# Kernel optimization log

Measured on AMD Instinct MI355X. Metric: run time of the kernel, lower is better.

Reference implementation:

```python
import jax, jax.numpy as jnp
import numpy as np

B, L, DEPTH, W = 32, 256, 4, 32

def setup_inputs() -> dict:
    key = jax.random.key(0)
    ks = jax.random.split(key, 12)
    rn = lambda k, sh: jax.random.normal(k, sh, dtype=jnp.float32)
    return {
        "x": rn(ks[0], (B, L, L)),
        "ai": rn(ks[1], (W, 1)),
        "ao": rn(ks[2], (1, W)),
        "a": rn(ks[3], (DEPTH, W, W)),
        "bi": rn(ks[4], (W, 1)),
        "bo": rn(ks[5], (1, W)),
        "b": rn(ks[6], (DEPTH, W, W)),
        "ci": rn(ks[7], (W, 1)),
        "co": rn(ks[8], (1, W)),
        "c": rn(ks[9], (DEPTH, W, W)),
        "bias_i": rn(ks[10], (W,)),
        "bias": rn(ks[11], (DEPTH, W)),
    }

def _layer(x, wc, wb, wa, bias):
    # x: [b, ci, X, Y]; wc/wb/wa: [co, ci]; circular 3x3 stencil via rolls
    y = jnp.einsum('oi,bixy->boxy', wc, x)
    nb = (jnp.roll(x, 1, axis=2) + jnp.roll(x, -1, axis=2)
          + jnp.roll(x, 1, axis=3) + jnp.roll(x, -1, axis=3))
    y = y + jnp.einsum('oi,bixy->boxy', wb, nb)
    dg = (jnp.roll(x, (1, 1), axis=(2, 3)) + jnp.roll(x, (-1, -1), axis=(2, 3))
          + jnp.roll(x, (1, -1), axis=(2, 3)) + jnp.roll(x, (-1, 1), axis=(2, 3)))
    y = y + jnp.einsum('oi,bixy->boxy', wa, dg)
    if bias is not None:
        y = y + bias[None, :, None, None]
    return y

def _act(x):
    # torch nn.GELU() default is exact (erf-based)
    return jax.nn.gelu(x, approximate=False)

def _func(x, ai, ao, a, bi, bo, b, ci, co, c, bias_i, bias):
    h = x[:, None, :, :]                       # [b,1,L,L]
    h = _act(_layer(h, ci, bi, ai, bias_i))    # [b,W,L,L]
    for k in range(a.shape[0]):
        h = _act(_layer(h, c[k], b[k], a[k], bias[k]))
    y = _layer(h, co, bo, ao, None)            # [b,1,L,L]
    return jnp.squeeze(y, axis=1)              # [b,L,L]

def reference(x, ai, ao, a, bi, bo, b, ci, co, c, bias_i, bias):
    f = lambda v: _func(v, ai, ao, a, bi, bo, b, ci, co, c, bias_i, bias)
    return 0.5 * (f(x) - f(-x))
```

## Files before the change

### kernel.cpp

```cpp
#include <hip/hip_runtime.h>
#include <hip/hip_bf16.h>

#define B_ 32
#define L_ 256
#define W_ 32
#define TILE 16
#define PSTR 40
#define LL (L_*L_)

typedef float    floatx4 __attribute__((ext_vector_type(4)));
typedef short    shortx8 __attribute__((ext_vector_type(8)));
typedef unsigned uintx2  __attribute__((ext_vector_type(2)));
typedef unsigned uintx4  __attribute__((ext_vector_type(4)));

__device__ __forceinline__ float gelu_fast(float x) {
    float x2 = x * x;
    float inner = fmaf(0.044715f * x2, x, x);
    float e = __builtin_amdgcn_exp2f(inner * -2.3022082299446597f);
    return x * __builtin_amdgcn_rcpf(1.0f + e);
}

#if __has_builtin(__builtin_amdgcn_cvt_pk_bf16_f32)
__device__ __forceinline__ unsigned pack_bf2(float a, float b) {
    auto v = __builtin_amdgcn_cvt_pk_bf16_f32(a, b);
    return __builtin_bit_cast(unsigned, v);
}
#else
__device__ __forceinline__ unsigned pack_bf2(float a, float b) {
    unsigned ua = __float_as_uint(a);
    unsigned ub = __float_as_uint(b);
    ua += 0x7fffu + ((ua >> 16) & 1u);
    ub += 0x7fffu + ((ub >> 16) & 1u);
    return (ua >> 16) | (ub & 0xffff0000u);
}
#endif

__device__ __forceinline__ int swizzle_blk(int p) {
    return (p & 7) * 1024 + (p >> 3);
}

__device__ __forceinline__ void conv9(
        const shortx8& t00, const shortx8& t01, const shortx8& t02,
        const shortx8& t10, const shortx8& t11, const shortx8& t12,
        const shortx8& t20, const shortx8& t21, const shortx8& t22,
        const shortx8 af[3][2], const float bv[2][4], floatx4 acc[2]) {
    #pragma unroll
    for (int h = 0; h < 2; ++h) {
        acc[h] = floatx4{bv[h][0], bv[h][1], bv[h][2], bv[h][3]};
        acc[h] = __builtin_amdgcn_mfma_f32_16x16x32_bf16(af[0][h], t11, acc[h], 0, 0, 0);
        acc[h] = __builtin_amdgcn_mfma_f32_16x16x32_bf16(af[1][h], t01, acc[h], 0, 0, 0);
        acc[h] = __builtin_amdgcn_mfma_f32_16x16x32_bf16(af[1][h], t21, acc[h], 0, 0, 0);
        acc[h] = __builtin_amdgcn_mfma_f32_16x16x32_bf16(af[1][h], t10, acc[h], 0, 0, 0);
        acc[h] = __builtin_amdgcn_mfma_f32_16x16x32_bf16(af[1][h], t12, acc[h], 0, 0, 0);
        acc[h] = __builtin_amdgcn_mfma_f32_16x16x32_bf16(af[2][h], t00, acc[h], 0, 0, 0);
        acc[h] = __builtin_amdgcn_mfma_f32_16x16x32_bf16(af[2][h], t02, acc[h], 0, 0, 0);
        acc[h] = __builtin_amdgcn_mfma_f32_16x16x32_bf16(af[2][h], t20, acc[h], 0, 0, 0);
        acc[h] = __builtin_amdgcn_mfma_f32_16x16x32_bf16(af[2][h], t22, acc[h], 0, 0, 0);
    }
}

__device__ __forceinline__ void gelu_pack4(const floatx4 acc[2], unsigned d[4]) {
    d[0] = pack_bf2(gelu_fast(acc[0][0]), gelu_fast(acc[0][1]));
    d[1] = pack_bf2(gelu_fast(acc[0][2]), gelu_fast(acc[0][3]));
    d[2] = pack_bf2(gelu_fast(acc[1][0]), gelu_fast(acc[1][1]));
    d[3] = pack_bf2(gelu_fast(acc[1][2]), gelu_fast(acc[1][3]));
}

__device__ __forceinline__ void build_afrag(
        const float* wc, const float* wb, const float* wa, const float* bias,
        int m, int q, shortx8 af[3][2], float bv[2][4]) {
    const float* wm[3] = { wc, wb, wa };
    #pragma unroll
    for (int f = 0; f < 3; ++f)
      #pragma unroll
      for (int h = 0; h < 2; ++h) {
        const float* row = wm[f] + (h*16 + m) * W_ + q*8;
        floatx4 r0 = *(const floatx4*)(row);
        floatx4 r1 = *(const floatx4*)(row + 4);
        union { shortx8 s; unsigned u[4]; } w;
        w.u[0] = pack_bf2(r0.x, r0.y);
        w.u[1] = pack_bf2(r0.z, r0.w);
        w.u[2] = pack_bf2(r1.x, r1.y);
        w.u[3] = pack_bf2(r1.z, r1.w);
        af[f][h] = w.s;
      }
    #pragma unroll
    for (int h = 0; h < 2; ++h)
      #pragma unroll
      for (int r = 0; r < 4; ++r)
        bv[h][r] = bias[h*16 + q*4 + r];
}

__global__ __launch_bounds__(256) void kern_first(
        const float* __restrict__ x, float scale,
        const float* __restrict__ ci, const float* __restrict__ bi,
        const float* __restrict__ ai, const float* __restrict__ bias_i,
        unsigned short* __restrict__ hout) {
    __shared__ float tile[18*18];
    __shared__ float wC[W_], wB[W_], wA[W_], bs[W_];
    int blk = swizzle_blk(blockIdx.x);
    int b = blk >> 8;
    int t = blk & 255;
    int x0 = (t >> 4) * TILE;
    int y0 = (t & 15) * TILE;
    int tid = threadIdx.x;
    if (tid < W_) { wC[tid] = ci[tid]; wB[tid] = bi[tid]; wA[tid] = ai[tid]; bs[tid] = bias_i[tid]; }
    const float* xb = x + (size_t)b * LL;
    for (int idx = tid; idx < 18*18; idx += 256) {
        int dy = idx / 18, dx = idx % 18;
        int gx = (x0 + dy - 1) & 255;
        int gy = (y0 + dx - 1) & 255;
        tile[idx] = scale * xb[gx * L_ + gy];
    }
    __syncthreads();
    int dx = tid & 15, dy = tid >> 4;
    const float* c0 = &tile[dy * 18 + dx];
    float ctr = c0[19];
    float nb  = c0[1] + c0[37] + c0[18] + c0[20];
    float dg  = c0[0] + c0[2] + c0[36] + c0[38];
    unsigned od[16];
    #pragma unroll
    for (int o = 0; o < 16; ++o) {
        float v0 = gelu_fast(wC[2*o]*ctr + wB[2*o]*nb + wA[2*o]*dg + bs[2*o]);
        float v1 = gelu_fast(wC[2*o+1]*ctr + wB[2*o+1]*nb + wA[2*o+1]*dg + bs[2*o+1]);
        od[o] = pack_bf2(v0, v1);
    }
    unsigned* dst = (unsigned*)(hout + (((((size_t)b << 8) | (unsigned)(x0+dy)) << 8 | (unsigned)(y0+dx)) << 5));
    *(uintx4*)(dst)      = uintx4{od[0],  od[1],  od[2],  od[3]};
    *(uintx4*)(dst + 4)  = uintx4{od[4],  od[5],  od[6],  od[7]};
    *(uintx4*)(dst + 8)  = uintx4{od[8],  od[9],  od[10], od[11]};
    *(uintx4*)(dst + 12) = uintx4{od[12], od[13], od[14], od[15]};
}

__global__ __launch_bounds__(256, 4) void kern_mid2(
        const unsigned short* __restrict__ hin,
        const float* __restrict__ wc1, const float* __restrict__ wb1,
        const float* __restrict__ wa1, const float* __restrict__ bias1,
        const float* __restrict__ wc2, const float* __restrict__ wb2,
        const float* __restrict__ wa2, const float* __restrict__ bias2,
        unsigned short* __restrict__ hout) {
    __shared__ unsigned short tile2[400 * PSTR];

    const int tid = threadIdx.x;
    const int blk = swizzle_blk(blockIdx.x);
    const int b  = blk >> 8;
    const int t  = blk & 255;
    const int x0 = (t >> 4) * TILE;
    const int y0 = (t & 15) * TILE;

    const unsigned short* hb = hin + ((size_t)b << 21);

    #pragma unroll
    for (int jj = 0; jj < 7; ++jj) {
        int j = tid + jj * 256;
        if (j < 1600) {
            int qtr = j & 3;
            int pos = j >> 2;
            int r = (pos * 3277) >> 16;
            int c = pos - r * 20;
            int gx = (x0 + r - 2) & 255;
            int gy = (y0 + c - 2) & 255;
            shortx8 v = *(const shortx8*)(hb + ((((unsigned)gx << 8) | (unsigned)gy) << 5) + qtr*8);
            *(shortx8*)(tile2 + pos * PSTR + qtr * 8) = v;
        }
    }

    const int lane = tid & 63;
    const int wv   = tid >> 6;
    const int m    = lane & 15;
    const int q    = lane >> 4;

    shortx8 afrag[3][2];
    float bv[2][4];
    build_afrag(wc1, wb1, wa1, bias1, m, q, afrag, bv);

    __syncthreads();

#define LDT(tr, off) (*(const shortx8*)(tile2 + (((tr)*20 + m + (off)))*PSTR + q*8))

    const int trow0 = wv * 4;
    shortx8 W[3][3];
    #pragma unroll
    for (int i = 0; i < 3; ++i) {
        W[i][0] = LDT(trow0 + i, 0);
        W[i][1] = LDT(trow0 + i, 1);
        W[i][2] = LDT(trow0 + i, 2);
    }
    unsigned heldA[2][4];
    #pragma unroll
    for (int rr = 0; rr < 4; ++rr) {
        const int top = rr % 3, mid = (rr + 1) % 3, bot = (rr + 2) % 3;
        floatx4 acc[2];
        conv9(W[top][0], W[top][1], W[top][2],
              W[mid][0], W[mid][1], W[mid][2],
              W[bot][0], W[bot][1], W[bot][2], afrag, bv, acc);
        unsigned d[4];
        gelu_pack4(acc, d);
        if (rr < 2) {
            heldA[rr][0] = d[0]; heldA[rr][1] = d[1];
            heldA[rr][2] = d[2]; heldA[rr][3] = d[3];
        } else {
            unsigned short* wp = tile2 + ((trow0 + rr)*20 + m)*PSTR + q*4;
            *(uintx2*)(wp)      = uintx2{d[0], d[1]};
            *(uintx2*)(wp + 16) = uintx2{d[2], d[3]};
        }
        if (rr < 3) {
            W[top][0] = LDT(trow0 + rr + 3, 0);
            W[top][1] = LDT(trow0 + rr + 3, 1);
            W[top][2] = LDT(trow0 + rr + 3, 2);
        }
    }

    int er0, ec0;
    if (wv == 0)      { er0 = 16; ec0 = m;  }
    else if (wv == 1) { er0 = 17; ec0 = m;  }
    else if (wv == 2) { er0 = m;  ec0 = 16; }
    else              { er0 = m;  ec0 = 17; }
    unsigned heldE[4];
    {
        shortx8 T[3][3];
        #pragma unroll
        for (int i = 0; i < 3; ++i)
          #pragma unroll
          for (int o = 0; o < 3; ++o)
            T[i][o] = *(const shortx8*)(tile2 + ((er0 + i)*20 + ec0 + o)*PSTR + q*8);
        floatx4 acc[2];
        conv9(T[0][0], T[0][1], T[0][2], T[1][0], T[1][1], T[1][2],
              T[2][0], T[2][1], T[2][2], afrag, bv, acc);
        gelu_pack4(acc, heldE);
    }
    const int heldEoff = (er0*20 + ec0)*PSTR + q*4;

    unsigned heldC[4];
    int heldCoff = 0;
    if (wv == 2) {
        int sr = 16 + ((m >> 1) & 1);
        int sc = 16 + (m & 1);
        shortx8 T[3][3];
        #pragma unroll
        for (int i = 0; i < 3; ++i)
          #pragma unroll
          for (int o = 0; o < 3; ++o)
            T[i][o] = *(const shortx8*)(tile2 + ((sr + i)*20 + sc + o)*PSTR + q*8);
        floatx4 acc[2];
        conv9(T[0][0], T[0][1], T[0][2], T[1][0], T[1][1], T[1][2],
              T[2][0], T[2][1], T[2][2], afrag, bv, acc);
        gelu_pack4(acc, heldC);
        heldCoff = (sr*20 + sc)*PSTR + q*4;
    }

    __syncthreads();

    #pragma unroll
    for (int rr = 0; rr < 2; ++rr) {
        unsigned short* wp = tile2 + ((trow0 + rr)*20 + m)*PSTR + q*4;
        *(uintx2*)(wp)      = uintx2{heldA[rr][0], heldA[rr][1]};
        *(uintx2*)(wp + 16) = uintx2{heldA[rr][2], heldA[rr][3]};
    }
    {
        unsigned short* wp = tile2 + heldEoff;
        *(uintx2*)(wp)      = uintx2{heldE[0], heldE[1]};
        *(uintx2*)(wp + 16) = uintx2{heldE[2], heldE[3]};
    }
    if (wv == 2 && m < 4) {
        unsigned short* wp = tile2 + heldCoff;
        *(uintx2*)(wp)      = uintx2{heldC[0], heldC[1]};
        *(uintx2*)(wp + 16) = uintx2{heldC[2], heldC[3]};
    }

    build_afrag(wc2, wb2, wa2, bias2, m, q, afrag, bv);

    __syncthreads();

    unsigned short* outb = hout + ((size_t)b << 21);
    #pragma unroll
    for (int i = 0; i < 3; ++i) {
        W[i][0] = LDT(trow0 + i, 0);
        W[i][1] = LDT(trow0 + i, 1);
        W[i][2] = LDT(trow0 + i, 2);
    }
    #pragma unroll
    for (int rr = 0; rr < 4; ++rr) {
        const int top = rr % 3, mid = (rr + 1) % 3, bot = (rr + 2) % 3;
        floatx4 acc[2];
        conv9(W[top][0], W[top][1], W[top][2],
              W[mid][0], W[mid][1], W[mid][2],
              W[bot][0], W[bot][1], W[bot][2], afrag, bv, acc);
        unsigned d[4];
        gelu_pack4(acc, d);
        unsigned short* dst = outb + ((((unsigned)(x0 + trow0 + rr) << 8) | (unsigned)(y0 + m)) << 5) + q*4;
        *(uintx2*)(dst)      = uintx2{d[0], d[1]};
        *(uintx2*)(dst + 16) = uintx2{d[2], d[3]};
        if (rr < 3) {
            W[top][0] = LDT(trow0 + rr + 3, 0);
            W[top][1] = LDT(trow0 + rr + 3, 1);
            W[top][2] = LDT(trow0 + rr + 3, 2);
        }
    }
#undef LDT
}

__global__ __launch_bounds__(256, 6) void kern_last(
        const unsigned short* __restrict__ hin,
        const float* __restrict__ co, const float* __restrict__ bo,
        const float* __restrict__ ao,
        float* __restrict__ out, int mode) {
    __shared__ unsigned short tile2[324 * PSTR];
    const int tid = threadIdx.x;
    const int blk = swizzle_blk(blockIdx.x);
    const int b  = blk >> 8;
    const int t  = blk & 255;
    const int x0 = (t >> 4) * TILE;
    const int y0 = (t & 15) * TILE;

    const unsigned short* hb = hin + ((size_t)b << 21);
    #pragma unroll
    for (int jj = 0; jj < 6; ++jj) {
        int j = tid + jj * 256;
        if (j < 1296) {
            int qtr = j & 3;
            int pos = j >> 2;
            int r = (pos * 3641) >> 16;
            int c = pos - r * 18;
            int gx = (x0 + r - 1) & 255;
            int gy = (y0 + c - 1) & 255;
            shortx8 v = *(const shortx8*)(hb + ((((unsigned)gx << 8) | (unsigned)gy) << 5) + qtr*8);
            *(shortx8*)(tile2 + pos * PSTR + qtr * 8) = v;
        }
    }

    const int lane = tid & 63;
    const int wv   = tid >> 6;
    const int m    = lane & 15;
    const int q    = lane >> 4;

    const float* wm[3] = { co, bo, ao };
    shortx8 afl[3];
    float z = (m == 0) ? 1.0f : 0.0f;
    #pragma unroll
    for (int f = 0; f < 3; ++f) {
        const float* row = wm[f] + q*8;
        floatx4 r0 = *(const floatx4*)(row);
        floatx4 r1 = *(const floatx4*)(row + 4);
        union { shortx8 s; unsigned u[4]; } w;
        w.u[0] = pack_bf2(r0.x * z, r0.y * z);
        w.u[1] = pack_bf2(r0.z * z, r0.w * z);
        w.u[2] = pack_bf2(r1.x * z, r1.y * z);
        w.u[3] = pack_bf2(r1.z * z, r1.w * z);
        afl[f] = w.s;
    }

    __syncthreads();

#define LDT18(tr, off) (*(const shortx8*)(tile2 + (((tr)*18 + m + (off)))*PSTR + q*8))
    const int trow0 = wv * 4;
    shortx8 W[3][3];
    #pragma unroll
    for (int i = 0; i < 3; ++i) {
        W[i][0] = LDT18(trow0 + i, 0);
        W[i][1] = LDT18(trow0 + i, 1);
        W[i][2] = LDT18(trow0 + i, 2);
    }
    #pragma unroll
    for (int rr = 0; rr < 4; ++rr) {
        const int top = rr % 3, mid = (rr + 1) % 3, bot = (rr + 2) % 3;
        floatx4 acc = {0.f, 0.f, 0.f, 0.f};
        acc = __builtin_amdgcn_mfma_f32_16x16x32_bf16(afl[0], W[mid][1], acc, 0, 0, 0);
        acc = __builtin_amdgcn_mfma_f32_16x16x32_bf16(afl[1], W[top][1], acc, 0, 0, 0);
        acc = __builtin_amdgcn_mfma_f32_16x16x32_bf16(afl[1], W[bot][1], acc, 0, 0, 0);
        acc = __builtin_amdgcn_mfma_f32_16x16x32_bf16(afl[1], W[mid][0], acc, 0, 0, 0);
        acc = __builtin_amdgcn_mfma_f32_16x16x32_bf16(afl[1], W[mid][2], acc, 0, 0, 0);
        acc = __builtin_amdgcn_mfma_f32_16x16x32_bf16(afl[2], W[top][0], acc, 0, 0, 0);
        acc = __builtin_amdgcn_mfma_f32_16x16x32_bf16(afl[2], W[top][2], acc, 0, 0, 0);
        acc = __builtin_amdgcn_mfma_f32_16x16x32_bf16(afl[2], W[bot][0], acc, 0, 0, 0);
        acc = __builtin_amdgcn_mfma_f32_16x16x32_bf16(afl[2], W[bot][2], acc, 0, 0, 0);
        if (q == 0) {
            size_t oidx = (size_t)b * LL + (size_t)(x0 + trow0 + rr) * L_ + (y0 + m);
            float v = 0.5f * acc[0];
            if (mode == 0) out[oidx] = v;
            else           out[oidx] = out[oidx] - v;
        }
        if (rr < 3) {
            W[top][0] = LDT18(trow0 + rr + 3, 0);
            W[top][1] = LDT18(trow0 + rr + 3, 1);
            W[top][2] = LDT18(trow0 + rr + 3, 2);
        }
    }
#undef LDT18
}

extern "C" void kernel_launch(void* const* d_in, const int* in_sizes, int n_in,
                              void* d_out, int out_size, void* d_ws, size_t ws_size,
                              hipStream_t stream) {
    const float* x      = (const float*)d_in[0];
    const float* ai     = (const float*)d_in[1];
    const float* ao     = (const float*)d_in[2];
    const float* a      = (const float*)d_in[3];
    const float* bi     = (const float*)d_in[4];
    const float* bo     = (const float*)d_in[5];
    const float* b      = (const float*)d_in[6];
    const float* ci     = (const float*)d_in[7];
    const float* co     = (const float*)d_in[8];
    const float* c      = (const float*)d_in[9];
    const float* bias_i = (const float*)d_in[10];
    const float* bias   = (const float*)d_in[11];
    float* out = (float*)d_out;

    const size_t elems = (size_t)B_ * W_ * LL;
    unsigned short* hA = (unsigned short*)d_ws;
    unsigned short* hB = hA + elems;

    dim3 grid(B_ * 256), blk(256);
    const int WW = W_ * W_;
    for (int s = 0; s < 2; ++s) {
        float scale = s ? -1.0f : 1.0f;
        kern_first<<<grid, blk, 0, stream>>>(x, scale, ci, bi, ai, bias_i, hA);
        kern_mid2<<<grid, blk, 0, stream>>>(hA,
            c, b, a, bias,
            c + WW, b + WW, a + WW, bias + W_,
            hB);
        kern_mid2<<<grid, blk, 0, stream>>>(hB,
            c + 2*WW, b + 2*WW, a + 2*WW, bias + 2*W_,
            c + 3*WW, b + 3*WW, a + 3*WW, bias + 3*W_,
            hA);
        kern_last<<<grid, blk, 0, stream>>>(hA, co, bo, ao, out, s);
    }
}
```

Baseline: 779.9 us.

## Fuse network into two kernels with halo recompute and merged sign passes

Restructures the eight-launch pipeline into two kernels. The front kernel computes the first layer directly from x in shared memory, with a wider halo, and feeds it straight into two mid layers. Both signs (x and -x) run in one grid, writing separate workspace halves. The back kernel reads a 3-pixel halo and fuses the remaining two mid layers with the output layer, looping over both signs and combining them in registers. This removes two intermediate activation round-trips through HBM, the read-modify-write on the output, and several launches, at the cost of redundant halo recompute and more shared memory per block.

```diff
diff --git a/kernel.cpp b/kernel.cpp
--- a/kernel.cpp
+++ b/kernel.cpp
@@ -7,6 +7,7 @@
 #define TILE 16
 #define PSTR 40
 #define LL (L_*L_)
+#define ELEMS ((size_t)B_ * W_ * LL)
 
 typedef float    floatx4 __attribute__((ext_vector_type(4)));
 typedef short    shortx8 __attribute__((ext_vector_type(8)));
@@ -91,77 +92,67 @@
         bv[h][r] = bias[h*16 + q*4 + r];
 }
 
-__global__ __launch_bounds__(256) void kern_first(
-        const float* __restrict__ x, float scale,
+__global__ __launch_bounds__(256, 4) void kern_front(
+        const float* __restrict__ x,
         const float* __restrict__ ci, const float* __restrict__ bi,
         const float* __restrict__ ai, const float* __restrict__ bias_i,
-        unsigned short* __restrict__ hout) {
-    __shared__ float tile[18*18];
-    __shared__ float wC[W_], wB[W_], wA[W_], bs[W_];
-    int blk = swizzle_blk(blockIdx.x);
-    int b = blk >> 8;
-    int t = blk & 255;
-    int x0 = (t >> 4) * TILE;
-    int y0 = (t & 15) * TILE;
-    int tid = threadIdx.x;
-    if (tid < W_) { wC[tid] = ci[tid]; wB[tid] = bi[tid]; wA[tid] = ai[tid]; bs[tid] = bias_i[tid]; }
-    const float* xb = x + (size_t)b * LL;
-    for (int idx = tid; idx < 18*18; idx += 256) {
-        int dy = idx / 18, dx = idx % 18;
-        int gx = (x0 + dy - 1) & 255;
-        int gy = (y0 + dx - 1) & 255;
-        tile[idx] = scale * xb[gx * L_ + gy];
-    }
-    __syncthreads();
-    int dx = tid & 15, dy = tid >> 4;
-    const float* c0 = &tile[dy * 18 + dx];
-    float ctr = c0[19];
-    float nb  = c0[1] + c0[37] + c0[18] + c0[20];
-    float dg  = c0[0] + c0[2] + c0[36] + c0[38];
-    unsigned od[16];
-    #pragma unroll
-    for (int o = 0; o < 16; ++o) {
-        float v0 = gelu_fast(wC[2*o]*ctr + wB[2*o]*nb + wA[2*o]*dg + bs[2*o]);
-        float v1 = gelu_fast(wC[2*o+1]*ctr + wB[2*o+1]*nb + wA[2*o+1]*dg + bs[2*o+1]);
-        od[o] = pack_bf2(v0, v1);
-    }
-    unsigned* dst = (unsigned*)(hout + (((((size_t)b << 8) | (unsigned)(x0+dy)) << 8 | (unsigned)(y0+dx)) << 5));
-    *(uintx4*)(dst)      = uintx4{od[0],  od[1],  od[2],  od[3]};
-    *(uintx4*)(dst + 4)  = uintx4{od[4],  od[5],  od[6],  od[7]};
-    *(uintx4*)(dst + 8)  = uintx4{od[8],  od[9],  od[10], od[11]};
-    *(uintx4*)(dst + 12) = uintx4{od[12], od[13], od[14], od[15]};
-}
-
-__global__ __launch_bounds__(256, 4) void kern_mid2(
-        const unsigned short* __restrict__ hin,
         const float* __restrict__ wc1, const float* __restrict__ wb1,
         const float* __restrict__ wa1, const float* __restrict__ bias1,
         const float* __restrict__ wc2, const float* __restrict__ wb2,
         const float* __restrict__ wa2, const float* __restrict__ bias2,
-        unsigned short* __restrict__ hout) {
+        unsigned short* __restrict__ hbase) {
     __shared__ unsigned short tile2[400 * PSTR];
+    __shared__ float xs[22 * 23];
+    __shared__ float wC[W_], wB[W_], wA[W_], bs[W_];
 
     const int tid = threadIdx.x;
-    const int blk = swizzle_blk(blockIdx.x);
+    const int raw = blockIdx.x;
+    const int s   = raw >> 13;
+    const int blk = swizzle_blk(raw & 8191);
     const int b  = blk >> 8;
     const int t  = blk & 255;
     const int x0 = (t >> 4) * TILE;
     const int y0 = (t & 15) * TILE;
-
-    const unsigned short* hb = hin + ((size_t)b << 21);
-
-    #pragma unroll
-    for (int jj = 0; jj < 7; ++jj) {
-        int j = tid + jj * 256;
-        if (j < 1600) {
-            int qtr = j & 3;
-            int pos = j >> 2;
-            int r = (pos * 3277) >> 16;
-            int c = pos - r * 20;
-            int gx = (x0 + r - 2) & 255;
-            int gy = (y0 + c - 2) & 255;
-            shortx8 v = *(const shortx8*)(hb + ((((unsigned)gx << 8) | (unsigned)gy) << 5) + qtr*8);
-            *(shortx8*)(tile2 + pos * PSTR + qtr * 8) = v;
+    const float scale = s ? -1.0f : 1.0f;
+
+    if (tid < W_) { wC[tid] = ci[tid]; wB[tid] = bi[tid]; wA[tid] = ai[tid]; bs[tid] = bias_i[tid]; }
+
+    const float* xb = x + (size_t)b * LL;
+    #pragma unroll
+    for (int ss = 0; ss < 2; ++ss) {
+        int idx = tid + ss * 256;
+        if (idx < 484) {
+            int r = (idx * 2979) >> 16;
+            int c = idx - r * 22;
+            int gx = (x0 + r - 3) & 255;
+            int gy = (y0 + c - 3) & 255;
+            xs[r * 23 + c] = scale * xb[gx * L_ + gy];
+        }
+    }
+    __syncthreads();
+
+    #pragma unroll
+    for (int ss = 0; ss < 2; ++ss) {
+        int idx = tid + ss * 256;
+        if (idx < 400) {
+            int i = (idx * 3277) >> 16;
+            int j = idx - i * 20;
+            const float* p0 = &xs[i * 23 + j];
+            float ctr = p0[24];
+            float nb  = p0[1] + p0[47] + p0[23] + p0[25];
+            float dg  = p0[0] + p0[2] + p0[46] + p0[48];
+            unsigned od[16];
+            #pragma unroll
+            for (int o = 0; o < 16; ++o) {
+                float v0 = gelu_fast(wC[2*o]*ctr + wB[2*o]*nb + wA[2*o]*dg + bs[2*o]);
+                float v1 = gelu_fast(wC[2*o+1]*ctr + wB[2*o+1]*nb + wA[2*o+1]*dg + bs[2*o+1]);
+                od[o] = pack_bf2(v0, v1);
+            }
+            unsigned* dst = (unsigned*)(tile2 + idx * PSTR);
+            *(uintx4*)(dst)      = uintx4{od[0],  od[1],  od[2],  od[3]};
+            *(uintx4*)(dst + 4)  = uintx4{od[4],  od[5],  od[6],  od[7]};
+            *(uintx4*)(dst + 8)  = uintx4{od[8],  od[9],  od[10], od[11]};
+            *(uintx4*)(dst + 12) = uintx4{od[12], od[13], od[14], od[15]};
         }
     }
 
@@ -272,7 +263,7 @@
 
     __syncthreads();
 
-    unsigned short* outb = hout + ((size_t)b << 21);
+    unsigned short* outb = hbase + (size_t)s * ELEMS + ((size_t)b << 21);
     #pragma unroll
     for (int i = 0; i < 3; ++i) {
         W[i][0] = LDT(trow0 + i, 0);
@@ -300,12 +291,17 @@
 #undef LDT
 }
 
-__global__ __launch_bounds__(256, 6) void kern_last(
-        const unsigned short* __restrict__ hin,
+__global__ __launch_bounds__(256, 4) void kern_back(
+        const unsigned short* __restrict__ hbase,
+        const float* __restrict__ wc1, const float* __restrict__ wb1,
+        const float* __restrict__ wa1, const float* __restrict__ bias1,
+        const float* __restrict__ wc2, const float* __restrict__ wb2,
+        const float* __restrict__ wa2, const float* __restrict__ bias2,
         const float* __restrict__ co, const float* __restrict__ bo,
         const float* __restrict__ ao,
-        float* __restrict__ out, int mode) {
-    __shared__ unsigned short tile2[324 * PSTR];
+        float* __restrict__ out) {
+    __shared__ unsigned short tile2[484 * PSTR];
+
     const int tid = threadIdx.x;
     const int blk = swizzle_blk(blockIdx.x);
     const int b  = blk >> 8;
@@ -313,80 +309,268 @@
     const int x0 = (t >> 4) * TILE;
     const int y0 = (t & 15) * TILE;
 
-    const unsigned short* hb = hin + ((size_t)b << 21);
-    #pragma unroll
-    for (int jj = 0; jj < 6; ++jj) {
-        int j = tid + jj * 256;
-        if (j < 1296) {
-            int qtr = j & 3;
-            int pos = j >> 2;
-            int r = (pos * 3641) >> 16;
-            int c = pos - r * 18;
-            int gx = (x0 + r - 1) & 255;
-            int gy = (y0 + c - 1) & 255;
-            shortx8 v = *(const shortx8*)(hb + ((((unsigned)gx << 8) | (unsigned)gy) << 5) + qtr*8);
-            *(shortx8*)(tile2 + pos * PSTR + qtr * 8) = v;
-        }
-    }
-
     const int lane = tid & 63;
     const int wv   = tid >> 6;
     const int m    = lane & 15;
     const int q    = lane >> 4;
 
-    const float* wm[3] = { co, bo, ao };
     shortx8 afl[3];
-    float z = (m == 0) ? 1.0f : 0.0f;
-    #pragma unroll
-    for (int f = 0; f < 3; ++f) {
-        const float* row = wm[f] + q*8;
-        floatx4 r0 = *(const floatx4*)(row);
-        floatx4 r1 = *(const floatx4*)(row + 4);
-        union { shortx8 s; unsigned u[4]; } w;
-        w.u[0] = pack_bf2(r0.x * z, r0.y * z);
-        w.u[1] = pack_bf2(r0.z * z, r0.w * z);
-        w.u[2] = pack_bf2(r1.x * z, r1.y * z);
-        w.u[3] = pack_bf2(r1.z * z, r1.w * z);
-        afl[f] = w.s;
-    }
-
-    __syncthreads();
-
-#define LDT18(tr, off) (*(const shortx8*)(tile2 + (((tr)*18 + m + (off)))*PSTR + q*8))
-    const int trow0 = wv * 4;
-    shortx8 W[3][3];
-    #pragma unroll
-    for (int i = 0; i < 3; ++i) {
-        W[i][0] = LDT18(trow0 + i, 0);
-        W[i][1] = LDT18(trow0 + i, 1);
-        W[i][2] = LDT18(trow0 + i, 2);
-    }
-    #pragma unroll
-    for (int rr = 0; rr < 4; ++rr) {
-        const int top = rr % 3, mid = (rr + 1) % 3, bot = (rr + 2) % 3;
-        floatx4 acc = {0.f, 0.f, 0.f, 0.f};
-        acc = __builtin_amdgcn_mfma_f32_16x16x32_bf16(afl[0], W[mid][1], acc, 0, 0, 0);
-        acc = __builtin_amdgcn_mfma_f32_16x16x32_bf16(afl[1], W[top][1], acc, 0, 0, 0);
-        acc = __builtin_amdgcn_mfma_f32_16x16x32_bf16(afl[1], W[bot][1], acc, 0, 0, 0);
-        acc = __builtin_amdgcn_mfma_f32_16x16x32_bf16(afl[1], W[mid][0], acc, 0, 0, 0);
-        acc = __builtin_amdgcn_mfma_f32_16x16x32_bf16(afl[1], W[mid][2], acc, 0, 0, 0);
-        acc = __builtin_amdgcn_mfma_f32_16x16x32_bf16(afl[2], W[top][0], acc, 0, 0, 0);
-        acc = __builtin_amdgcn_mfma_f32_16x16x32_bf16(afl[2], W[top][2], acc, 0, 0, 0);
-        acc = __builtin_amdgcn_mfma_f32_16x16x32_bf16(afl[2], W[bot][0], acc, 0, 0, 0);
-        acc = __builtin_amdgcn_mfma_f32_16x16x32_bf16(afl[2], W[bot][2], acc, 0, 0, 0);
-        if (q == 0) {
-            size_t oidx = (size_t)b * LL + (size_t)(x0 + trow0 + rr) * L_ + (y0 + m);
-            float v = 0.5f * acc[0];
-            if (mode == 0) out[oidx] = v;
-            else           out[oidx] = out[oidx] - v;
-        }
-        if (rr < 3) {
-            W[top][0] = LDT18(trow0 + rr + 3, 0);
-            W[top][1] = LDT18(trow0 + rr + 3, 1);
-            W[top][2] = LDT18(trow0 + rr + 3, 2);
-        }
-    }
-#undef LDT18
+    {
+        const float* wm[3] = { co, bo, ao };
+        float z = (m == 0) ? 1.0f : 0.0f;
+        #pragma unroll
+        for (int f = 0; f < 3; ++f) {
+            const float* row = wm[f] + q*8;
+            floatx4 r0 = *(const floatx4*)(row);
+            floatx4 r1 = *(const floatx4*)(row + 4);
+            union { shortx8 s; unsigned u[4]; } w;
+            w.u[0] = pack_bf2(r0.x * z, r0.y * z);
+            w.u[1] = pack_bf2(r0.z * z, r0.w * z);
+            w.u[2] = pack_bf2(r1.x * z, r1.y * z);
+            w.u[3] = pack_bf2(r1.z * z, r1.w * z);
+            afl[f] = w.s;
+        }
+    }
+
+    float vkeep[4];
+
+#define LDT22(tr, off) (*(const shortx8*)(tile2 + (((tr)*22 + m + (off)))*PSTR + q*8))
+
+    for (int s = 0; s < 2; ++s) {
+        __syncthreads();
+
+        const unsigned short* hb = hbase + (size_t)s * ELEMS + ((size_t)b << 21);
+        #pragma unroll
+        for (int jj = 0; jj < 8; ++jj) {
+            int j = tid + jj * 256;
+            if (j < 1936) {
+                int qtr = j & 3;
+                int pos = j >> 2;
+                int r = (pos * 2979) >> 16;
+                int c = pos - r * 22;
+                int gx = (x0 + r - 3) & 255;
+                int gy = (y0 + c - 3) & 255;
+                shortx8 v = *(const shortx8*)(hb + ((((unsigned)gx << 8) | (unsigned)gy) << 5) + qtr*8);
+                *(shortx8*)(tile2 + pos * PSTR + qtr * 8) = v;
+            }
+        }
+
+        shortx8 afrag[3][2];
+        float bv[2][4];
+        build_afrag(wc1, wb1, wa1, bias1, m, q, afrag, bv);
+
+        __syncthreads();
+
+        const int r0 = wv * 5;
+        shortx8 W[3][3];
+        #pragma unroll
+        for (int i = 0; i < 3; ++i) {
+            W[i][0] = LDT22(r0 + i, 0);
+            W[i][1] = LDT22(r0 + i, 1);
+            W[i][2] = LDT22(r0 + i, 2);
+        }
+        unsigned heldM[2][4];
+        #pragma unroll
+        for (int rr = 0; rr < 5; ++rr) {
+            const int top = rr % 3, mid = (rr + 1) % 3, bot = (rr + 2) % 3;
+            floatx4 acc[2];
+            conv9(W[top][0], W[top][1], W[top][2],
+                  W[mid][0], W[mid][1], W[mid][2],
+                  W[bot][0], W[bot][1], W[bot][2], afrag, bv, acc);
+            unsigned d[4];
+            gelu_pack4(acc, d);
+            if (rr < 2) {
+                heldM[rr][0] = d[0]; heldM[rr][1] = d[1];
+                heldM[rr][2] = d[2]; heldM[rr][3] = d[3];
+            } else {
+                unsigned short* wp = tile2 + ((r0 + rr)*22 + m)*PSTR + q*4;
+                *(uintx2*)(wp)      = uintx2{d[0], d[1]};
+                *(uintx2*)(wp + 16) = uintx2{d[2], d[3]};
+            }
+            if (rr < 4) {
+                W[top][0] = LDT22(r0 + rr + 3, 0);
+                W[top][1] = LDT22(r0 + rr + 3, 1);
+                W[top][2] = LDT22(r0 + rr + 3, 2);
+            }
+        }
+
+        unsigned heldV[4];
+        const int ec = 16 + wv;
+        {
+            shortx8 T[3][3];
+            #pragma unroll
+            for (int i = 0; i < 3; ++i)
+              #pragma unroll
+              for (int o = 0; o < 3; ++o)
+                T[i][o] = *(const shortx8*)(tile2 + ((m + i)*22 + ec + o)*PSTR + q*8);
+            floatx4 acc[2];
+            conv9(T[0][0], T[0][1], T[0][2], T[1][0], T[1][1], T[1][2],
+                  T[2][0], T[2][1], T[2][2], afrag, bv, acc);
+            gelu_pack4(acc, heldV);
+        }
+
+        unsigned heldC[4];
+        const int sr_c = 16 + (m >> 2), sc_c = 16 + (m & 3);
+        if (wv == 0) {
+            shortx8 T[3][3];
+            #pragma unroll
+            for (int i = 0; i < 3; ++i)
+              #pragma unroll
+              for (int o = 0; o < 3; ++o)
+                T[i][o] = *(const shortx8*)(tile2 + ((sr_c + i)*22 + sc_c + o)*PSTR + q*8);
+            floatx4 acc[2];
+            conv9(T[0][0], T[0][1], T[0][2], T[1][0], T[1][1], T[1][2],
+                  T[2][0], T[2][1], T[2][2], afrag, bv, acc);
+            gelu_pack4(acc, heldC);
+        }
+
+        __syncthreads();
+
+        #pragma unroll
+        for (int rr = 0; rr < 2; ++rr) {
+            unsigned short* wp = tile2 + ((r0 + rr)*22 + m)*PSTR + q*4;
+            *(uintx2*)(wp)      = uintx2{heldM[rr][0], heldM[rr][1]};
+            *(uintx2*)(wp + 16) = uintx2{heldM[rr][2], heldM[rr][3]};
+        }
+        {
+            unsigned short* wp = tile2 + (m*22 + ec)*PSTR + q*4;
+            *(uintx2*)(wp)      = uintx2{heldV[0], heldV[1]};
+            *(uintx2*)(wp + 16) = uintx2{heldV[2], heldV[3]};
+        }
+        if (wv == 0) {
+            unsigned short* wp = tile2 + (sr_c*22 + sc_c)*PSTR + q*4;
+            *(uintx2*)(wp)      = uintx2{heldC[0], heldC[1]};
+            *(uintx2*)(wp + 16) = uintx2{heldC[2], heldC[3]};
+        }
+
+        build_afrag(wc2, wb2, wa2, bias2, m, q, afrag, bv);
+
+        __syncthreads();
+
+        const int trow0 = wv * 4;
+        #pragma unroll
+        for (int i = 0; i < 3; ++i) {
+            W[i][0] = LDT22(trow0 + i, 0);
+            W[i][1] = LDT22(trow0 + i, 1);
+            W[i][2] = LDT22(trow0 + i, 2);
+        }
+        unsigned heldA[2][4];
+        #pragma unroll
+        for (int rr = 0; rr < 4; ++rr) {
+            const int top = rr % 3, mid = (rr + 1) % 3, bot = (rr + 2) % 3;
+            floatx4 acc[2];
+            conv9(W[top][0], W[top][1], W[top][2],
+                  W[mid][0], W[mid][1], W[mid][2],
+                  W[bot][0], W[bot][1], W[bot][2], afrag, bv, acc);
+            unsigned d[4];
+            gelu_pack4(acc, d);
+            if (rr < 2) {
+                heldA[rr][0] = d[0]; heldA[rr][1] = d[1];
+                heldA[rr][2] = d[2]; heldA[rr][3] = d[3];
+            } else {
+                unsigned short* wp = tile2 + ((trow0 + rr)*22 + m)*PSTR + q*4;
+                *(uintx2*)(wp)      = uintx2{d[0], d[1]};
+                *(uintx2*)(wp + 16) = uintx2{d[2], d[3]};
+            }
+            if (rr < 3) {
+                W[top][0] = LDT22(trow0 + rr + 3, 0);
+                W[top][1] = LDT22(trow0 + rr + 3, 1);
+                W[top][2] = LDT22(trow0 + rr + 3, 2);
+            }
+        }
+
+        int er0, ec0;
+        if (wv == 0)      { er0 = 16; ec0 = m;  }
+        else if (wv == 1) { er0 = 17; ec0 = m;  }
+        else if (wv == 2) { er0 = m;  ec0 = 16; }
+        else              { er0 = m;  ec0 = 17; }
+        unsigned heldE[4];
+        {
+            shortx8 T[3][3];
+            #pragma unroll
+            for (int i = 0; i < 3; ++i)
+              #pragma unroll
+              for (int o = 0; o < 3; ++o)
+                T[i][o] = *(const shortx8*)(tile2 + ((er0 + i)*22 + ec0 + o)*PSTR + q*8);
+            floatx4 acc[2];
+            conv9(T[0][0], T[0][1], T[0][2], T[1][0], T[1][1], T[1][2],
+                  T[2][0], T[2][1], T[2][2], afrag, bv, acc);
+            gelu_pack4(acc, heldE);
+        }
+        const int heldEoff = (er0*22 + ec0)*PSTR + q*4;
+
+        unsigned heldC2[4];
+        int heldC2off = 0;
+        if (wv == 2) {
+            int sr = 16 + ((m >> 1) & 1);
+            int sc = 16 + (m & 1);
+            shortx8 T[3][3];
+            #pragma unroll
+            for (int i = 0; i < 3; ++i)
+              #pragma unroll
+              for (int o = 0; o < 3; ++o)
+                T[i][o] = *(const shortx8*)(tile2 + ((sr + i)*22 + sc + o)*PSTR + q*8);
+            floatx4 acc[2];
+            conv9(T[0][0], T[0][1], T[0][2], T[1][0], T[1][1], T[1][2],
+                  T[2][0], T[2][1], T[2][2], afrag, bv, acc);
+            gelu_pack4(acc, heldC2);
+            heldC2off = (sr*22 + sc)*PSTR + q*4;
+        }
+
+        __syncthreads();
+
+        #pragma unroll
+        for (int rr = 0; rr < 2; ++rr) {
+            unsigned short* wp = tile2 + ((trow0 + rr)*22 + m)*PSTR + q*4;
+            *(uintx2*)(wp)      = uintx2{heldA[rr][0], heldA[rr][1]};
+            *(uintx2*)(wp + 16) = uintx2{heldA[rr][2], heldA[rr][3]};
+        }
+        {
+            unsigned short* wp = tile2 + heldEoff;
+            *(uintx2*)(wp)      = uintx2{heldE[0], heldE[1]};
+            *(uintx2*)(wp + 16) = uintx2{heldE[2], heldE[3]};
+        }
+        if (wv == 2 && m < 4) {
+            unsigned short* wp = tile2 + heldC2off;
+            *(uintx2*)(wp)      = uintx2{heldC2[0], heldC2[1]};
+            *(uintx2*)(wp + 16) = uintx2{heldC2[2], heldC2[3]};
+        }
+
+        __syncthreads();
+
+        #pragma unroll
+        for (int i = 0; i < 3; ++i) {
+            W[i][0] = LDT22(trow0 + i, 0);
+            W[i][1] = LDT22(trow0 + i, 1);
+            W[i][2] = LDT22(trow0 + i, 2);
+        }
+        #pragma unroll
+        for (int rr = 0; rr < 4; ++rr) {
+            const int top = rr % 3, mid = (rr + 1) % 3, bot = (rr + 2) % 3;
+            floatx4 acc = {0.f, 0.f, 0.f, 0.f};
+            acc = __builtin_amdgcn_mfma_f32_16x16x32_bf16(afl[0], W[mid][1], acc, 0, 0, 0);
+            acc = __builtin_amdgcn_mfma_f32_16x16x32_bf16(afl[1], W[top][1], acc, 0, 0, 0);
+            acc = __builtin_amdgcn_mfma_f32_16x16x32_bf16(afl[1], W[bot][1], acc, 0, 0, 0);
+            acc = __builtin_amdgcn_mfma_f32_16x16x32_bf16(afl[1], W[mid][0], acc, 0, 0, 0);
+            acc = __builtin_amdgcn_mfma_f32_16x16x32_bf16(afl[1], W[mid][2], acc, 0, 0, 0);
+            acc = __builtin_amdgcn_mfma_f32_16x16x32_bf16(afl[2], W[top][0], acc, 0, 0, 0);
+            acc = __builtin_amdgcn_mfma_f32_16x16x32_bf16(afl[2], W[top][2], acc, 0, 0, 0);
+            acc = __builtin_amdgcn_mfma_f32_16x16x32_bf16(afl[2], W[bot][0], acc, 0, 0, 0);
+            acc = __builtin_amdgcn_mfma_f32_16x16x32_bf16(afl[2], W[bot][2], acc, 0, 0, 0);
+            if (s == 0) {
+                vkeep[rr] = acc[0];
+            } else if (q == 0) {
+                size_t oidx = (size_t)b * LL + (size_t)(x0 + trow0 + rr) * L_ + (y0 + m);
+                out[oidx] = 0.5f * (vkeep[rr] - acc[0]);
+            }
+            if (rr < 3) {
+                W[top][0] = LDT22(trow0 + rr + 3, 0);
+                W[top][1] = LDT22(trow0 + rr + 3, 1);
+                W[top][2] = LDT22(trow0 + rr + 3, 2);
+            }
+        }
+    }
+#undef LDT22
 }
 
 extern "C" void kernel_launch(void* const* d_in, const int* in_sizes, int n_in,
@@ -406,23 +590,17 @@
     const float* bias   = (const float*)d_in[11];
     float* out = (float*)d_out;
 
-    const size_t elems = (size_t)B_ * W_ * LL;
     unsigned short* hA = (unsigned short*)d_ws;
-    unsigned short* hB = hA + elems;
-
-    dim3 grid(B_ * 256), blk(256);
+
     const int WW = W_ * W_;
-    for (int s = 0; s < 2; ++s) {
-        float scale = s ? -1.0f : 1.0f;
-        kern_first<<<grid, blk, 0, stream>>>(x, scale, ci, bi, ai, bias_i, hA);
-        kern_mid2<<<grid, blk, 0, stream>>>(hA,
-            c, b, a, bias,
-            c + WW, b + WW, a + WW, bias + W_,
-            hB);
-        kern_mid2<<<grid, blk, 0, stream>>>(hB,
-            c + 2*WW, b + 2*WW, a + 2*WW, bias + 2*W_,
-            c + 3*WW, b + 3*WW, a + 3*WW, bias + 3*W_,
-            hA);
-        kern_last<<<grid, blk, 0, stream>>>(hA, co, bo, ao, out, s);
-    }
-}
+    kern_front<<<dim3(2 * B_ * 256), dim3(256), 0, stream>>>(
+        x, ci, bi, ai, bias_i,
+        c, b, a, bias,
+        c + WW, b + WW, a + WW, bias + W_,
+        hA);
+    kern_back<<<dim3(B_ * 256), dim3(256), 0, stream>>>(
+        hA,
+        c + 2*WW, b + 2*WW, a + 2*WW, bias + 2*W_,
+        c + 3*WW, b + 3*WW, a + 3*WW, bias + 3*W_,
+        co, bo, ao, out);
+}
```

Result: slower. 1.189 ms (+52.5%).
